# Kernel tuning notes

Hardware: AMD Instinct MI355X
Metric: run time of the kernel (lower is better)

Reference implementation:

```python
import jax, jax.numpy as jnp
import numpy as np

KSIZE = 13
PAD = KSIZE // 2
EPS = 1e-5
MIN_DISP = 1e-3  # clamp to avoid inf depth at zero disparity


def _unfold(x):
    # B,C,H,W -> B, C*k*k, H, W  (im2col with 'same' padding, stride 1; matches F.unfold)
    return jax.lax.conv_general_dilated_patches(
        x, filter_shape=(KSIZE, KSIZE), window_strides=(1, 1),
        padding=[(PAD, PAD), (PAD, PAD)])


def _znorm(p):
    # zero-mean, unit-norm over patch dim -> ZNCC becomes a plain dot product
    p = p - p.mean(axis=1, keepdims=True)
    return p / (jnp.linalg.norm(p, axis=1, keepdims=True) + EPS)


def setup_inputs() -> dict:
    key = jax.random.key(0)
    k1, k2 = jax.random.split(key)
    B, C, H, W = 1, 3, 192, 320
    l_image = jax.random.uniform(k1, (B, C, H, W), jnp.float32)
    # right image = horizontally shifted left + small noise so true matches exist
    r_image = jnp.roll(l_image, shift=-8, axis=-1) + 0.01 * jax.random.normal(k2, (B, C, H, W), jnp.float32)
    fx = 240.0
    intri = jnp.array([[[fx, 0.0, W / 2.0], [0.0, fx, H / 2.0], [0.0, 0.0, 1.0]]], jnp.float32)
    l_extri = jnp.eye(4, dtype=jnp.float32)[None]
    r_extri = l_extri.at[:, 0, 3].set(0.54)  # 0.54 m stereo baseline
    return {"l_image": l_image, "r_image": r_image, "l_intri": intri,
            "r_intri": intri, "l_extri": l_extri, "r_extri": r_extri}


def reference(l_image, r_image, l_intri, r_intri, l_extri, r_extri):
    B, C, H, W = l_image.shape
    # patch unfold (im2col) + ZNCC normalization
    ln = _znorm(_unfold(l_image).reshape(1, -1, H, W))  # 1,D,H,W
    rn = _znorm(_unfold(r_image).reshape(1, -1, H, W))
    # full-width correlation volume: each left pixel vs every right column in its row
    vol = jnp.einsum('bdhw,bdhv->bhwv', ln, rn)  # 1,H,W,W
    # reduce=True -> best-matching right column index
    corresp = jnp.argmax(vol, axis=-1).astype(l_image.dtype)  # 1,H,W
    disp = jnp.abs(corresp - jnp.arange(W, dtype=l_image.dtype))
    # disparity -> depth: depth = fx * baseline / disp
    fx = l_intri[:, 0, 0]
    rel = r_extri @ jnp.linalg.inv(l_extri)  # relative right<-left transform
    baseline = jnp.linalg.norm(rel[:, :3, 3], axis=-1)
    depth = fx[:, None, None] * baseline[:, None, None] / jnp.clip(disp, MIN_DISP, None)
    return depth
```

## Files before the change

kernel.cpp:

```cpp
#include <hip/hip_runtime.h>
#include <math.h>

#define HH 192
#define WW 320
#define DTOT 507.0f
#define KD 39
#define NSPAN 5
#define NCHUNK 5
#define XS 64
#define TV 64
#define TX 76
#define TU 80
#define TUW 76
#define TIS 76
#define TDIAG 77
#define NPIX (HH*WW)

__global__ void prep_kernel(const float* __restrict__ li, const float* __restrict__ le,
                            const float* __restrict__ re, float* __restrict__ sc,
                            unsigned long long* __restrict__ keys) {
    int t = blockIdx.x * blockDim.x + threadIdx.x;
    if (keys != nullptr && t < NPIX) keys[t] = 0ull;
    if (t == 0) {
        float a[4][4], inv[4][4];
        for (int i = 0; i < 4; ++i)
            for (int j = 0; j < 4; ++j) { a[i][j] = le[i*4+j]; inv[i][j] = (i == j) ? 1.0f : 0.0f; }
        for (int c = 0; c < 4; ++c) {
            int p = c; float mx = fabsf(a[c][c]);
            for (int r = c+1; r < 4; ++r) { float v = fabsf(a[r][c]); if (v > mx) { mx = v; p = r; } }
            if (p != c) for (int j = 0; j < 4; ++j) {
                float tq = a[c][j]; a[c][j] = a[p][j]; a[p][j] = tq;
                tq = inv[c][j]; inv[c][j] = inv[p][j]; inv[p][j] = tq;
            }
            float id = 1.0f / a[c][c];
            for (int j = 0; j < 4; ++j) { a[c][j] *= id; inv[c][j] *= id; }
            for (int r = 0; r < 4; ++r) if (r != c) {
                float f = a[r][c];
                for (int j = 0; j < 4; ++j) { a[r][j] -= f*a[c][j]; inv[r][j] -= f*inv[c][j]; }
            }
        }
        float rel[3];
        for (int i = 0; i < 3; ++i)
            rel[i] = re[i*4+0]*inv[0][3] + re[i*4+1]*inv[1][3] + re[i*4+2]*inv[2][3] + re[i*4+3]*inv[3][3];
        float baseline = sqrtf(rel[0]*rel[0] + rel[1]*rel[1] + rel[2]*rel[2]);
        sc[0] = li[0] * baseline;
    }
}

__global__ __launch_bounds__(256) void match_kernel(
        const float* __restrict__ limg, const float* __restrict__ rimg,
        unsigned long long* __restrict__ keys) {
    __shared__ float Ls[KD][TX];
    __shared__ float Rs[KD][TU];
    __shared__ float Tc[TU][TIS];
    __shared__ float colL[TX];
    __shared__ float colR1[TUW];
    __shared__ float colR2[TUW];
    __shared__ float smuR[TV];
    __shared__ float sivR[TV];
    __shared__ float redS[4][XS];
    __shared__ int   redV[4][XS];

    const int span = blockIdx.x;
    const int h    = blockIdx.y;
    const int ch   = blockIdx.z;
    const int wlo  = span * XS;
    const int ulo  = ch * TV;
    const int tid  = threadIdx.x;
    const int lane = tid & 63;
    const int wave = tid >> 6;

    for (int i = tid; i < KD*TX; i += 256) {
        int k = i / TX, xl = i - k*TX;
        int c = k / 13, dy = k - c*13;
        int y = h - 6 + dy, x = wlo - 6 + xl;
        float v = 0.0f;
        if ((unsigned)y < (unsigned)HH && (unsigned)x < (unsigned)WW) v = limg[(c*HH + y)*WW + x];
        Ls[k][xl] = v;
    }
    for (int i = tid; i < KD*TU; i += 256) {
        int k = i / TU, uc = i - k*TU;
        int c = k / 13, dy = k - c*13;
        int y = h - 6 + dy, u = ulo - 6 + uc;
        float v = 0.0f;
        if ((unsigned)y < (unsigned)HH && (unsigned)u < (unsigned)WW) v = rimg[(c*HH + y)*WW + u];
        Rs[k][uc] = v;
    }
    __syncthreads();

    if (tid < TX) {
        float s = 0.0f;
        for (int k = 0; k < KD; ++k) s += Ls[k][tid];
        colL[tid] = s;
    } else if (tid >= 128 && tid < 128 + TUW) {
        int c = tid - 128;
        float s1 = 0.0f, s2 = 0.0f;
        for (int k = 0; k < KD; ++k) {
            float v = Rs[k][c];
            s1 += v;
            s2 = fmaf(v, v, s2);
        }
        colR1[c] = s1;
        colR2[c] = s2;
    }
    __syncthreads();

    float muL;
    {
        float s = 0.0f;
        #pragma unroll
        for (int dx = 0; dx < 13; ++dx) s += colL[lane + dx];
        muL = s / DTOT;
    }

    if (tid < 190) {
        const int ti = tid % 19, tj = tid / 19;
        const int i0 = ti * 4, j0 = tj * 8;
        float a[4][8];
        #pragma unroll
        for (int r = 0; r < 4; ++r)
            #pragma unroll
            for (int c = 0; c < 8; ++c) a[r][c] = 0.0f;
        for (int k = 0; k < KD; ++k) {
            float4 la = *(const float4*)&Ls[k][i0];
            float4 r0 = *(const float4*)&Rs[k][j0];
            float4 r1 = *(const float4*)&Rs[k][j0+4];
            float lx[4] = {la.x, la.y, la.z, la.w};
            float rx[8] = {r0.x, r0.y, r0.z, r0.w, r1.x, r1.y, r1.z, r1.w};
            #pragma unroll
            for (int r = 0; r < 4; ++r)
                #pragma unroll
                for (int c = 0; c < 8; ++c)
                    a[r][c] = fmaf(lx[r], rx[c], a[r][c]);
        }
        #pragma unroll
        for (int c = 0; c < 8; ++c) {
            *(float4*)&Tc[j0+c][i0] = make_float4(a[0][c], a[1][c], a[2][c], a[3][c]);
        }
    } else if (tid >= 192) {
        int vcc = tid - 192;
        float s1 = 0.0f, s2 = 0.0f;
        #pragma unroll
        for (int dx = 0; dx < 13; ++dx) { s1 += colR1[vcc + dx]; s2 += colR2[vcc + dx]; }
        float mu = s1 / DTOT;
        float var = fmaxf(s2 - s1*s1/DTOT, 0.0f);
        smuR[vcc] = mu;
        sivR[vcc] = 1.0f / (sqrtf(var) + 1e-5f);
    }
    __syncthreads();

    float best = -1e30f;
    int bestv = 0;
    const float dml = DTOT * muL;
    for (int vi = 0; vi < 16; ++vi) {
        int vc = wave * 16 + vi;
        const float* tp0 = &Tc[vc][0] + lane;
        float S = 0.0f;
        int boff = 0;
        #pragma unroll
        for (int g = 0; g < 3; ++g) {
            asm volatile("" : "+v"(boff));
            float y0 = tp0[boff];
            float y1 = tp0[boff + TDIAG];
            float y2 = tp0[boff + 2*TDIAG];
            float y3 = tp0[boff + 3*TDIAG];
            S += y0; S += y1; S += y2; S += y3;
            boff += 4*TDIAG;
        }
        S += tp0[12*TDIAG];
        float score = (S - dml * smuR[vc]) * sivR[vc];
        int v = ulo + vc;
        if (score > best) { best = score; bestv = v; }
    }

    redS[wave][lane] = best;
    redV[wave][lane] = bestv;
    __syncthreads();
    if (tid < XS) {
        float b = redS[0][tid]; int bv = redV[0][tid];
        for (int wv = 1; wv < 4; ++wv) {
            float s = redS[wv][tid]; int v2 = redV[wv][tid];
            if (s > b || (s == b && v2 < bv)) { b = s; bv = v2; }
        }
        unsigned ob = __float_as_uint(b);
        ob = (ob & 0x80000000u) ? ~ob : (ob | 0x80000000u);
        unsigned long long key = ((unsigned long long)ob << 32) | (unsigned)(~(unsigned)bv);
        atomicMax(&keys[h*WW + wlo + tid], key);
    }
}

__global__ __launch_bounds__(256) void depth_kernel(const unsigned long long* __restrict__ keys,
                                                    const float* __restrict__ sc,
                                                    float* __restrict__ out) {
    int t = blockIdx.x * 256 + threadIdx.x;
    unsigned long long k = keys[t];
    int v = (int)(~(unsigned int)k);
    float w = (float)(t % WW);
    float disp = fabsf((float)v - w);
    disp = fmaxf(disp, 0.001f);
    out[t] = sc[0] / disp;
}

__global__ __launch_bounds__(256) void match_fallback(
        const float* __restrict__ limg, const float* __restrict__ rimg,
        const float* __restrict__ ws, float* __restrict__ out) {
    __shared__ float Ls[KD][76];
    __shared__ float Rs[KD][76];
    __shared__ float Tt[76][81];
    __shared__ float colL[76];
    __shared__ float colR1[76];
    __shared__ float colR2[76];
    __shared__ float smuR[64];
    __shared__ float sivR[64];
    __shared__ float redS[4][64];
    __shared__ int   redV[4][64];

    const int span = blockIdx.x;
    const int h    = blockIdx.y;
    const int wlo  = span * 64;
    const int tid  = threadIdx.x;
    const int lane = tid & 63;
    const int wave = tid >> 6;

    for (int i = tid; i < KD*76; i += 256) {
        int k = i / 76, xl = i % 76;
        int c = k / 13, dy = k % 13;
        int y = h - 6 + dy, x = wlo - 6 + xl;
        float v = 0.0f;
        if (y >= 0 && y < HH && x >= 0 && x < WW) v = limg[(c*HH + y)*WW + x];
        Ls[k][xl] = v;
    }
    __syncthreads();

    if (tid < 76) {
        float s = 0.0f;
        for (int k = 0; k < KD; ++k) s += Ls[k][tid];
        colL[tid] = s;
    }
    __syncthreads();

    float muL;
    {
        float s = 0.0f;
        #pragma unroll
        for (int dx = 0; dx < 13; ++dx) s += colL[lane + dx];
        muL = s / DTOT;
    }

    float best = -1e30f;
    int bestv = 0;

    for (int ch = 0; ch < NCHUNK; ++ch) {
        const int ulo = ch * 64;
        for (int i = tid; i < KD*76; i += 256) {
            int k = i / 76, uc = i % 76;
            int c = k / 13, dy = k % 13;
            int y = h - 6 + dy, u = ulo - 6 + uc;
            float v = 0.0f;
            if (y >= 0 && y < HH && u >= 0 && u < WW) v = rimg[(c*HH + y)*WW + u];
            Rs[k][uc] = v;
        }
        __syncthreads();

        if (tid < 76) {
            float s1 = 0.0f, s2 = 0.0f;
            for (int k = 0; k < KD; ++k) {
                float v = Rs[k][tid];
                s1 += v;
                s2 = fmaf(v, v, s2);
            }
            colR1[tid] = s1;
            colR2[tid] = s2;
        }

        for (int t = tid; t < 361; t += 256) {
            int ti = t % 19, tj = t / 19;
            int i0 = ti * 4, j0 = tj * 4;
            float a00=0,a01=0,a02=0,a03=0, a10=0,a11=0,a12=0,a13=0;
            float a20=0,a21=0,a22=0,a23=0, a30=0,a31=0,a32=0,a33=0;
            for (int k = 0; k < KD; ++k) {
                float4 la = *(const float4*)&Ls[k][i0];
                float4 rb = *(const float4*)&Rs[k][j0];
                a00 = fmaf(la.x, rb.x, a00); a01 = fmaf(la.x, rb.y, a01);
                a02 = fmaf(la.x, rb.z, a02); a03 = fmaf(la.x, rb.w, a03);
                a10 = fmaf(la.y, rb.x, a10); a11 = fmaf(la.y, rb.y, a11);
                a12 = fmaf(la.y, rb.z, a12); a13 = fmaf(la.y, rb.w, a13);
                a20 = fmaf(la.z, rb.x, a20); a21 = fmaf(la.z, rb.y, a21);
                a22 = fmaf(la.z, rb.z, a22); a23 = fmaf(la.z, rb.w, a23);
                a30 = fmaf(la.w, rb.x, a30); a31 = fmaf(la.w, rb.y, a31);
                a32 = fmaf(la.w, rb.z, a32); a33 = fmaf(la.w, rb.w, a33);
            }
            float* tr0 = &Tt[i0+0][j0]; tr0[0]=a00; tr0[1]=a01; tr0[2]=a02; tr0[3]=a03;
            float* tr1 = &Tt[i0+1][j0]; tr1[0]=a10; tr1[1]=a11; tr1[2]=a12; tr1[3]=a13;
            float* tr2 = &Tt[i0+2][j0]; tr2[0]=a20; tr2[1]=a21; tr2[2]=a22; tr2[3]=a23;
            float* tr3 = &Tt[i0+3][j0]; tr3[0]=a30; tr3[1]=a31; tr3[2]=a32; tr3[3]=a33;
        }
        __syncthreads();

        if (tid < 64) {
            float s1 = 0.0f, s2 = 0.0f;
            #pragma unroll
            for (int dx = 0; dx < 13; ++dx) { s1 += colR1[tid + dx]; s2 += colR2[tid + dx]; }
            float mu = s1 / DTOT;
            float var = fmaxf(s2 - s1*s1/DTOT, 0.0f);
            smuR[tid] = mu;
            sivR[tid] = 1.0f / (sqrtf(var) + 1e-5f);
        }
        __syncthreads();

        for (int vi = 0; vi < 16; ++vi) {
            int vc = wave * 16 + vi;
            int v  = ulo + vc;
            const float* tp = &Tt[lane][vc];
            float S = 0.0f;
            #pragma unroll
            for (int dxp = 0; dxp < 13; ++dxp)
                S += tp[dxp * 82];
            float score = (S - DTOT * muL * smuR[vc]) * sivR[vc];
            if (score > best) { best = score; bestv = v; }
        }
    }

    redS[wave][lane] = best;
    redV[wave][lane] = bestv;
    __syncthreads();
    if (tid < 64) {
        float b = redS[0][tid]; int bv = redV[0][tid];
        for (int wv = 1; wv < 4; ++wv) {
            float s = redS[wv][tid]; int v2 = redV[wv][tid];
            if (s > b || (s == b && v2 < bv)) { b = s; bv = v2; }
        }
        int w = wlo + tid;
        float disp = fabsf((float)bv - (float)w);
        disp = fmaxf(disp, 0.001f);
        out[h*WW + w] = ws[0] / disp;
    }
}

extern "C" void kernel_launch(void* const* d_in, const int* in_sizes, int n_in,
                              void* d_out, int out_size, void* d_ws, size_t ws_size,
                              hipStream_t stream) {
    const float* limg   = (const float*)d_in[0];
    const float* rimg   = (const float*)d_in[1];
    const float* lintri = (const float*)d_in[2];
    const float* lex    = (const float*)d_in[4];
    const float* rex    = (const float*)d_in[5];
    float* out = (float*)d_out;
    float* scp = (float*)d_ws;

    const size_t need = 8 + (size_t)NPIX * 8;
    if (ws_size >= need) {
        unsigned long long* keys = (unsigned long long*)d_ws + 1;
        hipLaunchKernelGGL(prep_kernel, dim3(NPIX/256), dim3(256), 0, stream,
                           lintri, lex, rex, scp, keys);
        hipLaunchKernelGGL(match_kernel, dim3(NSPAN, HH, NCHUNK), dim3(256), 0, stream,
                           limg, rimg, keys);
        hipLaunchKernelGGL(depth_kernel, dim3(NPIX/256), dim3(256), 0, stream,
                           keys, scp, out);
    } else {
        hipLaunchKernelGGL(prep_kernel, dim3(1), dim3(64), 0, stream,
                           lintri, lex, rex, scp, (unsigned long long*)nullptr);
        hipLaunchKernelGGL(match_fallback, dim3(NSPAN, HH), dim3(256), 0, stream,
                           limg, rimg, scp, out);
    }
}
```

Before: 152.1 us.

## Split correlation tile into two half passes to shrink shared memory

The Tc correlation tile is computed in two halves of 40 right columns each, so Tc shrinks from 80 to 40 rows and total LDS per block drops, aiming for more resident blocks per CU. The column sums for the left and right windows move onto the otherwise idle waves 2 and 3 and run alongside the first GEMM half, which removes one barrier phase. Diagonals that straddle the two halves are carried as partial sums in registers. The final per-wave shared-memory reduction is replaced by four atomicMax calls per pixel, one from each wave. In exchange the block takes an extra barrier and loads unevenly, since waves 0-1 do all the GEMM work while waves 2-3 do the boundary diagonals.

```diff
diff --git a/kernel.cpp b/kernel.cpp
--- a/kernel.cpp
+++ b/kernel.cpp
@@ -9,11 +9,10 @@
 #define NCHUNK 5
 #define XS 64
 #define TV 64
-#define TX 76
-#define TU 80
-#define TUW 76
+#define TSX 80
+#define TJ 40
 #define TIS 76
-#define TDIAG 77
+#define TD2 77
 #define NPIX (HH*WW)
 
 __global__ void prep_kernel(const float* __restrict__ li, const float* __restrict__ le,
@@ -50,16 +49,14 @@
 __global__ __launch_bounds__(256) void match_kernel(
         const float* __restrict__ limg, const float* __restrict__ rimg,
         unsigned long long* __restrict__ keys) {
-    __shared__ float Ls[KD][TX];
-    __shared__ float Rs[KD][TU];
-    __shared__ float Tc[TU][TIS];
-    __shared__ float colL[TX];
-    __shared__ float colR1[TUW];
-    __shared__ float colR2[TUW];
+    __shared__ float Ls[KD][TSX];
+    __shared__ float Rs[KD][TSX];
+    __shared__ float Tc[TJ][TIS];
+    __shared__ float colL[TSX];
+    __shared__ float colR1[TSX];
+    __shared__ float colR2[TSX];
     __shared__ float smuR[TV];
     __shared__ float sivR[TV];
-    __shared__ float redS[4][XS];
-    __shared__ int   redV[4][XS];
 
     const int span = blockIdx.x;
     const int h    = blockIdx.y;
@@ -70,16 +67,16 @@
     const int lane = tid & 63;
     const int wave = tid >> 6;
 
-    for (int i = tid; i < KD*TX; i += 256) {
-        int k = i / TX, xl = i - k*TX;
+    for (int i = tid; i < KD*TSX; i += 256) {
+        int k = i / TSX, xl = i - k*TSX;
         int c = k / 13, dy = k - c*13;
         int y = h - 6 + dy, x = wlo - 6 + xl;
         float v = 0.0f;
         if ((unsigned)y < (unsigned)HH && (unsigned)x < (unsigned)WW) v = limg[(c*HH + y)*WW + x];
         Ls[k][xl] = v;
     }
-    for (int i = tid; i < KD*TU; i += 256) {
-        int k = i / TU, uc = i - k*TU;
+    for (int i = tid; i < KD*TSX; i += 256) {
+        int k = i / TSX, uc = i - k*TSX;
         int c = k / 13, dy = k - c*13;
         int y = h - 6 + dy, u = ulo - 6 + uc;
         float v = 0.0f;
@@ -88,20 +85,65 @@
     }
     __syncthreads();
 
-    if (tid < TX) {
-        float s = 0.0f;
-        for (int k = 0; k < KD; ++k) s += Ls[k][tid];
-        colL[tid] = s;
-    } else if (tid >= 128 && tid < 128 + TUW) {
-        int c = tid - 128;
-        float s1 = 0.0f, s2 = 0.0f;
-        for (int k = 0; k < KD; ++k) {
-            float v = Rs[k][c];
-            s1 += v;
-            s2 = fmaf(v, v, s2);
-        }
-        colR1[c] = s1;
-        colR2[c] = s2;
+    if (wave < 2) {
+        int t = (wave << 6) + lane;
+        if (t < 95) {
+            int ti = t % 19, tj = t / 19;
+            int i0 = 4*ti, j0 = 8*tj;
+            float a[4][8];
+            #pragma unroll
+            for (int r = 0; r < 4; ++r)
+                #pragma unroll
+                for (int c = 0; c < 8; ++c) a[r][c] = 0.0f;
+            for (int k = 0; k < KD; ++k) {
+                float4 la = *(const float4*)&Ls[k][i0];
+                float4 r0 = *(const float4*)&Rs[k][j0];
+                float4 r1 = *(const float4*)&Rs[k][j0+4];
+                float lx[4] = {la.x, la.y, la.z, la.w};
+                float rx[8] = {r0.x, r0.y, r0.z, r0.w, r1.x, r1.y, r1.z, r1.w};
+                #pragma unroll
+                for (int r = 0; r < 4; ++r)
+                    #pragma unroll
+                    for (int c = 0; c < 8; ++c)
+                        a[r][c] = fmaf(lx[r], rx[c], a[r][c]);
+            }
+            #pragma unroll
+            for (int c = 0; c < 8; ++c)
+                *(float4*)&Tc[j0+c][i0] = make_float4(a[0][c], a[1][c], a[2][c], a[3][c]);
+        }
+    } else if (wave == 2) {
+        if (lane < 20) {
+            float sx = 0.0f, sy = 0.0f, sz = 0.0f, sw = 0.0f;
+            for (int k = 0; k < KD; ++k) {
+                float4 v = *(const float4*)&Ls[k][4*lane];
+                sx += v.x; sy += v.y; sz += v.z; sw += v.w;
+            }
+            *(float4*)&colL[4*lane] = make_float4(sx, sy, sz, sw);
+        }
+    } else {
+        if (lane < 20) {
+            float ax = 0.0f, ay = 0.0f, az = 0.0f, aw = 0.0f;
+            float bx = 0.0f, by = 0.0f, bz = 0.0f, bw = 0.0f;
+            for (int k = 0; k < KD; ++k) {
+                float4 v = *(const float4*)&Rs[k][4*lane];
+                ax += v.x; ay += v.y; az += v.z; aw += v.w;
+                bx = fmaf(v.x, v.x, bx); by = fmaf(v.y, v.y, by);
+                bz = fmaf(v.z, v.z, bz); bw = fmaf(v.w, v.w, bw);
+            }
+            *(float4*)&colR1[4*lane] = make_float4(ax, ay, az, aw);
+            *(float4*)&colR2[4*lane] = make_float4(bx, by, bz, bw);
+        }
+        asm volatile("s_waitcnt lgkmcnt(0)" ::: "memory");
+        {
+            int vc = lane;
+            float s1 = 0.0f, s2 = 0.0f;
+            #pragma unroll
+            for (int dx = 0; dx < 13; ++dx) { s1 += colR1[vc + dx]; s2 += colR2[vc + dx]; }
+            float mu = s1 / DTOT;
+            float var = fmaxf(s2 - s1*s1/DTOT, 0.0f);
+            smuR[vc] = mu;
+            sivR[vc] = 1.0f / (sqrtf(var) + 1e-5f);
+        }
     }
     __syncthreads();
 
@@ -112,81 +154,117 @@
         for (int dx = 0; dx < 13; ++dx) s += colL[lane + dx];
         muL = s / DTOT;
     }
-
-    if (tid < 190) {
-        const int ti = tid % 19, tj = tid / 19;
-        const int i0 = ti * 4, j0 = tj * 8;
-        float a[4][8];
+    const float dml = DTOT * muL;
+
+    float best = -1e30f;
+    int bestv = 0;
+    float Sp[10];
+
+    {
+        const int vb0 = wave * 10;
         #pragma unroll
-        for (int r = 0; r < 4; ++r)
-            #pragma unroll
-            for (int c = 0; c < 8; ++c) a[r][c] = 0.0f;
-        for (int k = 0; k < KD; ++k) {
-            float4 la = *(const float4*)&Ls[k][i0];
-            float4 r0 = *(const float4*)&Rs[k][j0];
-            float4 r1 = *(const float4*)&Rs[k][j0+4];
-            float lx[4] = {la.x, la.y, la.z, la.w};
-            float rx[8] = {r0.x, r0.y, r0.z, r0.w, r1.x, r1.y, r1.z, r1.w};
+        for (int s = 0; s < 10; ++s) {
+            int vc = vb0 + s;
+            if (vc < 28) {
+                const float* tp0 = &Tc[vc][0] + lane;
+                float S = 0.0f;
+                int boff = 0;
+                #pragma unroll
+                for (int g = 0; g < 3; ++g) {
+                    asm volatile("" : "+v"(boff));
+                    float y0 = tp0[boff];
+                    float y1 = tp0[boff + TD2];
+                    float y2 = tp0[boff + 2*TD2];
+                    float y3 = tp0[boff + 3*TD2];
+                    S += y0; S += y1; S += y2; S += y3;
+                    boff += 4*TD2;
+                }
+                S += tp0[12*TD2];
+                float score = (S - dml * smuR[vc]) * sivR[vc];
+                int v = ulo + vc;
+                if (score > best) { best = score; bestv = v; }
+            } else {
+                int dmax = 39 - vc;
+                float S = 0.0f;
+                for (int d = 0; d <= dmax; ++d) S += Tc[vc + d][lane + d];
+                Sp[s] = S;
+            }
+        }
+    }
+    __syncthreads();
+
+    if (wave < 2) {
+        int t = (wave << 6) + lane;
+        if (t < 95) {
+            int ti = t % 19, tj = t / 19;
+            int i0 = 4*ti, j0 = 8*tj;
+            float a[4][8];
             #pragma unroll
             for (int r = 0; r < 4; ++r)
                 #pragma unroll
-                for (int c = 0; c < 8; ++c)
-                    a[r][c] = fmaf(lx[r], rx[c], a[r][c]);
-        }
+                for (int c = 0; c < 8; ++c) a[r][c] = 0.0f;
+            for (int k = 0; k < KD; ++k) {
+                float4 la = *(const float4*)&Ls[k][i0];
+                float4 r0 = *(const float4*)&Rs[k][40 + j0];
+                float4 r1 = *(const float4*)&Rs[k][40 + j0 + 4];
+                float lx[4] = {la.x, la.y, la.z, la.w};
+                float rx[8] = {r0.x, r0.y, r0.z, r0.w, r1.x, r1.y, r1.z, r1.w};
+                #pragma unroll
+                for (int r = 0; r < 4; ++r)
+                    #pragma unroll
+                    for (int c = 0; c < 8; ++c)
+                        a[r][c] = fmaf(lx[r], rx[c], a[r][c]);
+            }
+            #pragma unroll
+            for (int c = 0; c < 8; ++c)
+                *(float4*)&Tc[j0+c][i0] = make_float4(a[0][c], a[1][c], a[2][c], a[3][c]);
+        }
+    }
+    __syncthreads();
+
+    if (wave < 2) {
+        const int vb1 = 40 + wave * 12;
         #pragma unroll
-        for (int c = 0; c < 8; ++c) {
-            *(float4*)&Tc[j0+c][i0] = make_float4(a[0][c], a[1][c], a[2][c], a[3][c]);
-        }
-    } else if (tid >= 192) {
-        int vcc = tid - 192;
-        float s1 = 0.0f, s2 = 0.0f;
+        for (int s = 0; s < 12; ++s) {
+            int vc = vb1 + s;
+            const float* tp0 = &Tc[vc - 40][0] + lane;
+            float S = 0.0f;
+            int boff = 0;
+            #pragma unroll
+            for (int g = 0; g < 3; ++g) {
+                asm volatile("" : "+v"(boff));
+                float y0 = tp0[boff];
+                float y1 = tp0[boff + TD2];
+                float y2 = tp0[boff + 2*TD2];
+                float y3 = tp0[boff + 3*TD2];
+                S += y0; S += y1; S += y2; S += y3;
+                boff += 4*TD2;
+            }
+            S += tp0[12*TD2];
+            float score = (S - dml * smuR[vc]) * sivR[vc];
+            int v = ulo + vc;
+            if (score > best) { best = score; bestv = v; }
+        }
+    } else {
+        const int vb0 = wave * 10;
         #pragma unroll
-        for (int dx = 0; dx < 13; ++dx) { s1 += colR1[vcc + dx]; s2 += colR2[vcc + dx]; }
-        float mu = s1 / DTOT;
-        float var = fmaxf(s2 - s1*s1/DTOT, 0.0f);
-        smuR[vcc] = mu;
-        sivR[vcc] = 1.0f / (sqrtf(var) + 1e-5f);
-    }
-    __syncthreads();
-
-    float best = -1e30f;
-    int bestv = 0;
-    const float dml = DTOT * muL;
-    for (int vi = 0; vi < 16; ++vi) {
-        int vc = wave * 16 + vi;
-        const float* tp0 = &Tc[vc][0] + lane;
-        float S = 0.0f;
-        int boff = 0;
-        #pragma unroll
-        for (int g = 0; g < 3; ++g) {
-            asm volatile("" : "+v"(boff));
-            float y0 = tp0[boff];
-            float y1 = tp0[boff + TDIAG];
-            float y2 = tp0[boff + 2*TDIAG];
-            float y3 = tp0[boff + 3*TDIAG];
-            S += y0; S += y1; S += y2; S += y3;
-            boff += 4*TDIAG;
-        }
-        S += tp0[12*TDIAG];
-        float score = (S - dml * smuR[vc]) * sivR[vc];
-        int v = ulo + vc;
-        if (score > best) { best = score; bestv = v; }
-    }
-
-    redS[wave][lane] = best;
-    redV[wave][lane] = bestv;
-    __syncthreads();
-    if (tid < XS) {
-        float b = redS[0][tid]; int bv = redV[0][tid];
-        for (int wv = 1; wv < 4; ++wv) {
-            float s = redS[wv][tid]; int v2 = redV[wv][tid];
-            if (s > b || (s == b && v2 < bv)) { b = s; bv = v2; }
-        }
-        unsigned ob = __float_as_uint(b);
-        ob = (ob & 0x80000000u) ? ~ob : (ob | 0x80000000u);
-        unsigned long long key = ((unsigned long long)ob << 32) | (unsigned)(~(unsigned)bv);
-        atomicMax(&keys[h*WW + wlo + tid], key);
-    }
+        for (int s = 0; s < 10; ++s) {
+            int vc = vb0 + s;
+            if (vc >= 28) {
+                float S = Sp[s];
+                int dstart = 40 - vc;
+                for (int d = dstart; d <= 12; ++d) S += Tc[vc + d - 40][lane + d];
+                float score = (S - dml * smuR[vc]) * sivR[vc];
+                int v = ulo + vc;
+                if (score > best) { best = score; bestv = v; }
+            }
+        }
+    }
+
+    unsigned ob = __float_as_uint(best);
+    ob = (ob & 0x80000000u) ? ~ob : (ob | 0x80000000u);
+    unsigned long long key = ((unsigned long long)ob << 32) | (unsigned)(~(unsigned)bestv);
+    atomicMax(&keys[h*WW + wlo + lane], key);
 }
 
 __global__ __launch_bounds__(256) void depth_kernel(const unsigned long long* __restrict__ keys,
```

After: 164.4 us. 8.1% more time.
